# Performance work log

Hardware: AMD Instinct MI355X
Metric: run time of the kernel (lower is better)

## Reference

```python
import jax, jax.numpy as jnp
import numpy as np

N_HEADS = 8
EMBED_DIM = 512
HEAD_DIM = EMBED_DIM // N_HEADS
INPUT_DIM = 512


def setup_inputs() -> dict:
    key = jax.random.key(0)
    ks = jax.random.split(key, 9)
    B, N = 4, 2048
    s_in = 1.0 / np.sqrt(INPUT_DIM)
    s_e = 1.0 / np.sqrt(EMBED_DIM)
    return {
        "q": jax.random.normal(ks[0], (B, N, INPUT_DIM), dtype=jnp.float32),
        "wq": jax.random.uniform(ks[1], (EMBED_DIM, INPUT_DIM), jnp.float32, -s_in, s_in),
        "bq": jax.random.uniform(ks[2], (EMBED_DIM,), jnp.float32, -s_in, s_in),
        "wk": jax.random.uniform(ks[3], (EMBED_DIM, INPUT_DIM), jnp.float32, -s_in, s_in),
        "bk": jax.random.uniform(ks[4], (EMBED_DIM,), jnp.float32, -s_in, s_in),
        "wv": jax.random.uniform(ks[5], (EMBED_DIM, INPUT_DIM), jnp.float32, -s_in, s_in),
        "bv": jax.random.uniform(ks[6], (EMBED_DIM,), jnp.float32, -s_in, s_in),
        "wo": jax.random.uniform(ks[7], (EMBED_DIM, EMBED_DIM), jnp.float32, -s_e, s_e),
        "bo": jax.random.uniform(ks[8], (EMBED_DIM,), jnp.float32, -s_e, s_e),
    }


def reference(q, wq, bq, wk, bk, wv, bv, wo, bo):
    B, N, _ = q.shape
    # linear projections (torch Linear: x @ W.T + b)
    Q = (q @ wq.T + bq).reshape(B, N, N_HEADS, HEAD_DIM).transpose(0, 2, 1, 3)
    K = (q @ wk.T + bk).reshape(B, N, N_HEADS, HEAD_DIM).transpose(0, 2, 1, 3)
    V = (q @ wv.T + bv).reshape(B, N, N_HEADS, HEAD_DIM).transpose(0, 2, 1, 3)
    scores = jnp.einsum("bhqd,bhkd->bhqk", Q, K) / jnp.sqrt(
        jnp.asarray(HEAD_DIM, dtype=q.dtype)
    )
    weights = jax.nn.softmax(scores, axis=-1)
    out = jnp.einsum("bhqk,bhkd->bhqd", weights, V)  # [B,H,N,Dh]
    out = out.transpose(0, 2, 1, 3).reshape(B, N, EMBED_DIM)
    return out @ wo.T + bo
```

## Files before the change

### kernel.cpp

```cpp
#include <hip/hip_runtime.h>
#include <hip/hip_bf16.h>
#include <math.h>

#define SEQ    2048
#define DH     64
#define EMB    512
#define INDIM  512
#define NHEADS 8
#define BATCH  4
#define MTOT   (BATCH * SEQ)

typedef __attribute__((ext_vector_type(8))) short bf16x8;
typedef __attribute__((ext_vector_type(4))) float f32x4;

__device__ __forceinline__ ushort f2bf(float x) {
  union { float f; unsigned u; } v; v.f = x;
  unsigned r = v.u + 0x7FFFu + ((v.u >> 16) & 1u);
  return (ushort)(r >> 16);
}

__device__ __forceinline__ unsigned cvt_pk_bf16(float lo, float hi) {
  unsigned r;
  asm("v_cvt_pk_bf16_f32 %0, %1, %2" : "=v"(r) : "v"(lo), "v"(hi));
  return r;
}

__global__ __launch_bounds__(256) void conv_bf16(const float* __restrict__ src,
                                                 ushort* __restrict__ dst, int n8) {
  const int i = blockIdx.x * 256 + threadIdx.x;
  if (i >= n8) return;
  const float4 a = ((const float4*)src)[i * 2];
  const float4 b = ((const float4*)src)[i * 2 + 1];
  uint4 o;
  o.x = cvt_pk_bf16(a.x, a.y);
  o.y = cvt_pk_bf16(a.z, a.w);
  o.z = cvt_pk_bf16(b.x, b.y);
  o.w = cvt_pk_bf16(b.z, b.w);
  ((uint4*)dst)[i] = o;
}

__global__ __launch_bounds__(256) void conv_bf16_w4(
    const float* __restrict__ w0, const float* __restrict__ w1,
    const float* __restrict__ w2, const float* __restrict__ w3,
    ushort* __restrict__ dst, int n8per) {
  const int i = blockIdx.x * 256 + threadIdx.x;
  if (i >= n8per) return;
  const float* src = (blockIdx.y == 0) ? w0 : (blockIdx.y == 1) ? w1
                   : (blockIdx.y == 2) ? w2 : w3;
  ushort* d = dst + (size_t)blockIdx.y * n8per * 8;
  const float4 a = ((const float4*)src)[i * 2];
  const float4 b = ((const float4*)src)[i * 2 + 1];
  uint4 o;
  o.x = cvt_pk_bf16(a.x, a.y);
  o.y = cvt_pk_bf16(a.z, a.w);
  o.z = cvt_pk_bf16(b.x, b.y);
  o.w = cvt_pk_bf16(b.z, b.w);
  ((uint4*)d)[i] = o;
}

template <int MODE>
__global__ __launch_bounds__(256) void mfma_gemm(
    const ushort* __restrict__ A, const ushort* __restrict__ W,
    const float* __restrict__ b0, const float* __restrict__ b1,
    const float* __restrict__ b2,
    ushort* __restrict__ outQ, ushort* __restrict__ outK,
    ushort* __restrict__ outVT, float* __restrict__ outF) {
  __shared__ __align__(16) char smem[MODE == 0 ? 35840 : 16384];
  ushort* As = (ushort*)smem;
  ushort* Bs = (ushort*)(smem + 8192);
  ushort* Tl = (ushort*)smem;

  const int bm = blockIdx.x * 128;
  const int bn = blockIdx.y * 128;
  const int tid = threadIdx.x;
  const int wave = tid >> 6, lane = tid & 63;
  const int g = lane >> 4, ln = lane & 15;
  const int wr = wave >> 1, wc = wave & 1;

  f32x4 acc[4][4];
#pragma unroll
  for (int m = 0; m < 4; ++m)
#pragma unroll
    for (int n = 0; n < 4; ++n) acc[m][n] = (f32x4){0.f, 0.f, 0.f, 0.f};

  const size_t a_base = (size_t)(bm + wave * 16 + (lane >> 2)) * INDIM + (lane & 3) * 8;
  const size_t b_base = (size_t)(bn + wave * 16 + (lane >> 2)) * INDIM + (lane & 3) * 8;
  ushort* ldsA0 = As + wave * 512;
  ushort* ldsA1 = As + 2048 + wave * 512;
  ushort* ldsB0 = Bs + wave * 512;
  ushort* ldsB1 = Bs + 2048 + wave * 512;

  for (int k0 = 0; k0 < INDIM; k0 += 32) {
    __syncthreads();
    __builtin_amdgcn_global_load_lds(
        (const __attribute__((address_space(1))) void*)(A + a_base + k0),
        (__attribute__((address_space(3))) void*)ldsA0, 16, 0, 0);
    __builtin_amdgcn_global_load_lds(
        (const __attribute__((address_space(1))) void*)(A + a_base + 64 * INDIM + k0),
        (__attribute__((address_space(3))) void*)ldsA1, 16, 0, 0);
    __builtin_amdgcn_global_load_lds(
        (const __attribute__((address_space(1))) void*)(W + b_base + k0),
        (__attribute__((address_space(3))) void*)ldsB0, 16, 0, 0);
    __builtin_amdgcn_global_load_lds(
        (const __attribute__((address_space(1))) void*)(W + b_base + 64 * INDIM + k0),
        (__attribute__((address_space(3))) void*)ldsB1, 16, 0, 0);
    __syncthreads();

    bf16x8 af[4], bfv[4];
#pragma unroll
    for (int m = 0; m < 4; ++m)
      af[m] = *(const bf16x8*)&As[(64 * wr + 16 * m + ln) * 32 + 8 * g];
#pragma unroll
    for (int n = 0; n < 4; ++n)
      bfv[n] = *(const bf16x8*)&Bs[(64 * wc + 16 * n + ln) * 32 + 8 * g];
#pragma unroll
    for (int m = 0; m < 4; ++m)
#pragma unroll
      for (int n = 0; n < 4; ++n)
        acc[m][n] = __builtin_amdgcn_mfma_f32_16x16x32_bf16(af[m], bfv[n], acc[m][n], 0, 0, 0);
  }

  if (MODE == 1) {
#pragma unroll
    for (int n = 0; n < 4; ++n) {
      const int e = bn + 64 * wc + 16 * n + ln;
      const float bv = b0[e];
#pragma unroll
      for (int m = 0; m < 4; ++m)
#pragma unroll
        for (int r = 0; r < 4; ++r) {
          const int row = bm + 64 * wr + 16 * m + 4 * g + r;
          outF[(size_t)row * EMB + e] = acc[m][n][r] + bv;
        }
    }
    return;
  }

  const int which = bn >> 9;
  const float* bias = (which == 0) ? b0 : (which == 1) ? b1 : b2;

  if (which < 2) {
    const float scl = (which == 0) ? 0.18033688f : 1.0f;
    ushort* dst = (which == 0) ? outQ : outK;
#pragma unroll
    for (int n = 0; n < 4; ++n) {
      const int e = (bn & 511) + 64 * wc + 16 * n + ln;
      const float bv = bias[e];
      const int h = e >> 6, d = e & 63;
#pragma unroll
      for (int m = 0; m < 4; ++m)
#pragma unroll
        for (int r = 0; r < 4; ++r) {
          const int row = bm + 64 * wr + 16 * m + 4 * g + r;
          const int b = row >> 11, nn = row & (SEQ - 1);
          dst[(((size_t)(b * NHEADS + h) * SEQ) + nn) * DH + d] =
              f2bf((acc[m][n][r] + bv) * scl);
        }
    }
  } else {
    __syncthreads();
#pragma unroll
    for (int n = 0; n < 4; ++n) {
      const int cl = 64 * wc + 16 * n + ln;
      const float bv = bias[(bn & 511) + cl];
#pragma unroll
      for (int m = 0; m < 4; ++m)
#pragma unroll
        for (int r = 0; r < 4; ++r) {
          const int rl = 64 * wr + 16 * m + 4 * g + r;
          Tl[cl * 140 + rl] = f2bf(acc[m][n][r] + bv);
        }
    }
    __syncthreads();
    const int c = tid >> 1;
    const int rh = (tid & 1) * 64;
    const int e = (bn & 511) + c;
    const int h = e >> 6, d = e & 63;
    const int b = bm >> 11;
    const int nn0 = (bm & (SEQ - 1)) + rh;
    ushort* drow = outVT + (((size_t)(b * NHEADS + h) * DH) + d) * SEQ + nn0;
#pragma unroll
    for (int j = 0; j < 8; ++j)
      *(bf16x8*)&drow[j * 8] = *(const bf16x8*)&Tl[c * 140 + rh + j * 8];
  }
}

__global__ __launch_bounds__(256) void attn_mfma(const ushort* __restrict__ Q,
                                                 const ushort* __restrict__ K,
                                                 const ushort* __restrict__ VT,
                                                 ushort* __restrict__ O) {
  __shared__ __align__(16) ushort Kl[64 * 72];
  __shared__ __align__(16) ushort Vl[80 * 72];
  __shared__ __align__(16) ushort Pl[4][32 * 72];
  __shared__ float Sl[4][32];

  const int tid = threadIdx.x;
  const int wave = tid >> 6, lane = tid & 63;
  const int g = lane >> 4, ln = lane & 15;

  const int orig = blockIdx.y * gridDim.x + blockIdx.x;
  const int swz = (orig & 7) * 64 + (orig >> 3);
  const int bh = swz >> 4;
  const int qx = swz & 15;
  const int qbase = qx * 128 + wave * 32;

  for (int i = tid; i < 16 * 72; i += 256)
    Vl[64 * 72 + i] = (i < 72) ? (ushort)0x3F80 : (ushort)0;

  const ushort* Qb = Q + ((size_t)bh * SEQ + qbase) * DH;
  const ushort* Kb = K + (size_t)bh * SEQ * DH;
  const ushort* Vb = VT + (size_t)bh * DH * SEQ;

  const bf16x8 qfA0 = *(const bf16x8*)&Qb[ln * DH + 8 * g];
  const bf16x8 qfA1 = *(const bf16x8*)&Qb[ln * DH + 32 + 8 * g];
  const bf16x8 qfB0 = *(const bf16x8*)&Qb[(16 + ln) * DH + 8 * g];
  const bf16x8 qfB1 = *(const bf16x8*)&Qb[(16 + ln) * DH + 32 + 8 * g];

  f32x4 oaccA[5], oaccB[5];
#pragma unroll
  for (int t = 0; t < 5; ++t) {
    oaccA[t] = (f32x4){0.f, 0.f, 0.f, 0.f};
    oaccB[t] = (f32x4){0.f, 0.f, 0.f, 0.f};
  }

  const int skv = tid >> 3, sd = (tid & 7) * 8;
  const int dt = tid >> 2, kc = (tid & 3) * 8;

  bf16x8 k0v = *(const bf16x8*)&Kb[(size_t)skv * DH + sd];
  bf16x8 k1v = *(const bf16x8*)&Kb[(size_t)(32 + skv) * DH + sd];
  bf16x8 v0v = *(const bf16x8*)&Vb[(size_t)dt * SEQ + kc];
  bf16x8 v1v = *(const bf16x8*)&Vb[(size_t)dt * SEQ + 32 + kc];

  for (int kv0 = 0; kv0 < SEQ; kv0 += 64) {
    __syncthreads();
    *(bf16x8*)&Kl[skv * 72 + sd] = k0v;
    *(bf16x8*)&Kl[(32 + skv) * 72 + sd] = k1v;
    *(bf16x8*)&Vl[dt * 72 + kc] = v0v;
    *(bf16x8*)&Vl[dt * 72 + 32 + kc] = v1v;

    const int nxt = (kv0 + 64 < SEQ) ? kv0 + 64 : kv0;
    k0v = *(const bf16x8*)&Kb[(size_t)(nxt + skv) * DH + sd];
    k1v = *(const bf16x8*)&Kb[(size_t)(nxt + 32 + skv) * DH + sd];
    v0v = *(const bf16x8*)&Vb[(size_t)dt * SEQ + nxt + kc];
    v1v = *(const bf16x8*)&Vb[(size_t)dt * SEQ + nxt + 32 + kc];

    asm volatile("s_waitcnt lgkmcnt(0)" ::: "memory");
    __builtin_amdgcn_s_barrier();

    f32x4 saccA[4], saccB[4];
    __builtin_amdgcn_s_setprio(1);
#pragma unroll
    for (int t = 0; t < 4; ++t) {
      saccA[t] = (f32x4){0.f, 0.f, 0.f, 0.f};
      saccB[t] = (f32x4){0.f, 0.f, 0.f, 0.f};
      const bf16x8 ka0 = *(const bf16x8*)&Kl[(16 * t + ln) * 72 + 8 * g];
      const bf16x8 ka1 = *(const bf16x8*)&Kl[(16 * t + ln) * 72 + 32 + 8 * g];
      saccA[t] = __builtin_amdgcn_mfma_f32_16x16x32_bf16(ka0, qfA0, saccA[t], 0, 0, 0);
      saccA[t] = __builtin_amdgcn_mfma_f32_16x16x32_bf16(ka1, qfA1, saccA[t], 0, 0, 0);
      saccB[t] = __builtin_amdgcn_mfma_f32_16x16x32_bf16(ka0, qfB0, saccB[t], 0, 0, 0);
      saccB[t] = __builtin_amdgcn_mfma_f32_16x16x32_bf16(ka1, qfB1, saccB[t], 0, 0, 0);
    }
    __builtin_amdgcn_s_setprio(0);

    ushort* Pw = Pl[wave];
#pragma unroll
    for (int t = 0; t < 4; ++t) {
      uint2 pkA, pkB;
      pkA.x = cvt_pk_bf16(exp2f(saccA[t][0]), exp2f(saccA[t][1]));
      pkA.y = cvt_pk_bf16(exp2f(saccA[t][2]), exp2f(saccA[t][3]));
      pkB.x = cvt_pk_bf16(exp2f(saccB[t][0]), exp2f(saccB[t][1]));
      pkB.y = cvt_pk_bf16(exp2f(saccB[t][2]), exp2f(saccB[t][3]));
      *(uint2*)&Pw[ln * 72 + 16 * t + 4 * g] = pkA;
      *(uint2*)&Pw[(16 + ln) * 72 + 16 * t + 4 * g] = pkB;
    }

    __builtin_amdgcn_s_setprio(1);
#pragma unroll
    for (int c = 0; c < 2; ++c) {
      const bf16x8 paA = *(const bf16x8*)&Pw[ln * 72 + 32 * c + 8 * g];
      const bf16x8 paB = *(const bf16x8*)&Pw[(16 + ln) * 72 + 32 * c + 8 * g];
#pragma unroll
      for (int t = 0; t < 5; ++t) {
        const bf16x8 vb = *(const bf16x8*)&Vl[(16 * t + ln) * 72 + 32 * c + 8 * g];
        oaccA[t] = __builtin_amdgcn_mfma_f32_16x16x32_bf16(paA, vb, oaccA[t], 0, 0, 0);
        oaccB[t] = __builtin_amdgcn_mfma_f32_16x16x32_bf16(paB, vb, oaccB[t], 0, 0, 0);
      }
    }
    __builtin_amdgcn_s_setprio(0);
  }

  if (ln == 0) {
#pragma unroll
    for (int r = 0; r < 4; ++r) {
      Sl[wave][4 * g + r] = oaccA[4][r];
      Sl[wave][16 + 4 * g + r] = oaccB[4][r];
    }
  }
  const float invlA = 1.0f / Sl[wave][ln];
  const float invlB = 1.0f / Sl[wave][16 + ln];

  const int b = bh >> 3, h = bh & 7;
#pragma unroll
  for (int r = 0; r < 4; ++r) {
    const float irA = __shfl(invlA, 4 * g + r);
    const float irB = __shfl(invlB, 4 * g + r);
    ushort* opA = O + ((size_t)(b * SEQ) + qbase + 4 * g + r) * EMB + h * 64;
    ushort* opB = O + ((size_t)(b * SEQ) + qbase + 16 + 4 * g + r) * EMB + h * 64;
#pragma unroll
    for (int t = 0; t < 4; ++t) {
      opA[16 * t + ln] = f2bf(oaccA[t][r] * irA);
      opB[16 * t + ln] = f2bf(oaccB[t][r] * irB);
    }
  }
}

extern "C" void kernel_launch(void* const* d_in, const int* in_sizes, int n_in,
                              void* d_out, int out_size, void* d_ws, size_t ws_size,
                              hipStream_t stream) {
  const float* q  = (const float*)d_in[0];
  const float* wq = (const float*)d_in[1];
  const float* bq = (const float*)d_in[2];
  const float* wk = (const float*)d_in[3];
  const float* bk = (const float*)d_in[4];
  const float* wv = (const float*)d_in[5];
  const float* bv = (const float*)d_in[6];
  const float* wo = (const float*)d_in[7];
  const float* bo = (const float*)d_in[8];
  float* out = (float*)d_out;

  const size_t XSZ = (size_t)MTOT * INDIM;
  const size_t WSZ = (size_t)EMB * INDIM;
  const size_t QSZ = (size_t)BATCH * NHEADS * SEQ * DH;
  ushort* wsX = (ushort*)d_ws;
  ushort* wsW = wsX + XSZ;
  ushort* wsQ = wsW + 4 * WSZ;
  ushort* wsK = wsQ + QSZ;
  ushort* wsVT = wsK + QSZ;
  ushort* wsA = wsVT + QSZ;

  const dim3 blk(256);

  conv_bf16<<<dim3(XSZ / 8 / 256), blk, 0, stream>>>(q, wsX, XSZ / 8);
  conv_bf16_w4<<<dim3(WSZ / 8 / 256, 4), blk, 0, stream>>>(wq, wk, wv, wo, wsW, WSZ / 8);

  mfma_gemm<0><<<dim3(MTOT / 128, 1536 / 128), blk, 0, stream>>>(
      wsX, wsW, bq, bk, bv, wsQ, wsK, wsVT, nullptr);

  attn_mfma<<<dim3(SEQ / 128, BATCH * NHEADS), blk, 0, stream>>>(wsQ, wsK, wsVT, wsA);

  mfma_gemm<1><<<dim3(MTOT / 128, EMB / 128), blk, 0, stream>>>(
      wsA, wsW + 3 * WSZ, bo, nullptr, nullptr, nullptr, nullptr, nullptr, out);
}
```

Before: 115.0 us.

## Split attention KV range across two blocks with atomic partial-sum reduction

The attention grid doubles from 512 to 1024 blocks by giving each block half of the key/value sequence. Unnormalized outputs and row sums are accumulated into fp32 workspace buffers with atomicAdd, and a new normalize_o kernel divides and converts the result to bf16. This works without a running max because the softmax takes no max-subtraction. The aim is more parallelism to fill the GPU's compute units, paid for with a memset, float atomics over an 8192x512 buffer, and an extra kernel pass. The exp2f call is also swapped for a raw v_exp_f32 instruction.

```diff
diff --git a/kernel.cpp b/kernel.cpp
--- a/kernel.cpp
+++ b/kernel.cpp
@@ -22,6 +22,12 @@
 __device__ __forceinline__ unsigned cvt_pk_bf16(float lo, float hi) {
   unsigned r;
   asm("v_cvt_pk_bf16_f32 %0, %1, %2" : "=v"(r) : "v"(lo), "v"(hi));
+  return r;
+}
+
+__device__ __forceinline__ float fast_exp2(float x) {
+  float r;
+  asm("v_exp_f32 %0, %1" : "=v"(r) : "v"(x));
   return r;
 }
 
@@ -188,21 +194,24 @@
 __global__ __launch_bounds__(256) void attn_mfma(const ushort* __restrict__ Q,
                                                  const ushort* __restrict__ K,
                                                  const ushort* __restrict__ VT,
-                                                 ushort* __restrict__ O) {
+                                                 float* __restrict__ P,
+                                                 float* __restrict__ L) {
   __shared__ __align__(16) ushort Kl[64 * 72];
   __shared__ __align__(16) ushort Vl[80 * 72];
   __shared__ __align__(16) ushort Pl[4][32 * 72];
-  __shared__ float Sl[4][32];
 
   const int tid = threadIdx.x;
   const int wave = tid >> 6, lane = tid & 63;
   const int g = lane >> 4, ln = lane & 15;
 
   const int orig = blockIdx.y * gridDim.x + blockIdx.x;
-  const int swz = (orig & 7) * 64 + (orig >> 3);
-  const int bh = swz >> 4;
-  const int qx = swz & 15;
+  const int swz = (orig & 7) * 128 + (orig >> 3);
+  const int bh = swz >> 5;
+  const int sub = swz & 31;
+  const int qx = sub >> 1;
+  const int half = sub & 1;
   const int qbase = qx * 128 + wave * 32;
+  const int kvbeg = half << 10;
 
   for (int i = tid; i < 16 * 72; i += 256)
     Vl[64 * 72 + i] = (i < 72) ? (ushort)0x3F80 : (ushort)0;
@@ -226,23 +235,28 @@
   const int skv = tid >> 3, sd = (tid & 7) * 8;
   const int dt = tid >> 2, kc = (tid & 3) * 8;
 
-  bf16x8 k0v = *(const bf16x8*)&Kb[(size_t)skv * DH + sd];
-  bf16x8 k1v = *(const bf16x8*)&Kb[(size_t)(32 + skv) * DH + sd];
-  bf16x8 v0v = *(const bf16x8*)&Vb[(size_t)dt * SEQ + kc];
-  bf16x8 v1v = *(const bf16x8*)&Vb[(size_t)dt * SEQ + 32 + kc];
-
-  for (int kv0 = 0; kv0 < SEQ; kv0 += 64) {
+  const ushort* kp0 = Kb + (size_t)(kvbeg + skv) * DH + sd;
+  const ushort* kp1 = kp0 + 32 * DH;
+  const ushort* vp0 = Vb + (size_t)dt * SEQ + kvbeg + kc;
+  const ushort* vp1 = vp0 + 32;
+
+  bf16x8 k0v = *(const bf16x8*)kp0;
+  bf16x8 k1v = *(const bf16x8*)kp1;
+  bf16x8 v0v = *(const bf16x8*)vp0;
+  bf16x8 v1v = *(const bf16x8*)vp1;
+
+  for (int it = 0; it < 16; ++it) {
     __syncthreads();
     *(bf16x8*)&Kl[skv * 72 + sd] = k0v;
     *(bf16x8*)&Kl[(32 + skv) * 72 + sd] = k1v;
     *(bf16x8*)&Vl[dt * 72 + kc] = v0v;
     *(bf16x8*)&Vl[dt * 72 + 32 + kc] = v1v;
 
-    const int nxt = (kv0 + 64 < SEQ) ? kv0 + 64 : kv0;
-    k0v = *(const bf16x8*)&Kb[(size_t)(nxt + skv) * DH + sd];
-    k1v = *(const bf16x8*)&Kb[(size_t)(nxt + 32 + skv) * DH + sd];
-    v0v = *(const bf16x8*)&Vb[(size_t)dt * SEQ + nxt + kc];
-    v1v = *(const bf16x8*)&Vb[(size_t)dt * SEQ + nxt + 32 + kc];
+    kp0 += 64 * DH; kp1 += 64 * DH; vp0 += 64; vp1 += 64;
+    k0v = *(const bf16x8*)kp0;
+    k1v = *(const bf16x8*)kp1;
+    v0v = *(const bf16x8*)vp0;
+    v1v = *(const bf16x8*)vp1;
 
     asm volatile("s_waitcnt lgkmcnt(0)" ::: "memory");
     __builtin_amdgcn_s_barrier();
@@ -266,10 +280,10 @@
 #pragma unroll
     for (int t = 0; t < 4; ++t) {
       uint2 pkA, pkB;
-      pkA.x = cvt_pk_bf16(exp2f(saccA[t][0]), exp2f(saccA[t][1]));
-      pkA.y = cvt_pk_bf16(exp2f(saccA[t][2]), exp2f(saccA[t][3]));
-      pkB.x = cvt_pk_bf16(exp2f(saccB[t][0]), exp2f(saccB[t][1]));
-      pkB.y = cvt_pk_bf16(exp2f(saccB[t][2]), exp2f(saccB[t][3]));
+      pkA.x = cvt_pk_bf16(fast_exp2(saccA[t][0]), fast_exp2(saccA[t][1]));
+      pkA.y = cvt_pk_bf16(fast_exp2(saccA[t][2]), fast_exp2(saccA[t][3]));
+      pkB.x = cvt_pk_bf16(fast_exp2(saccB[t][0]), fast_exp2(saccB[t][1]));
+      pkB.y = cvt_pk_bf16(fast_exp2(saccB[t][2]), fast_exp2(saccB[t][3]));
       *(uint2*)&Pw[ln * 72 + 16 * t + 4 * g] = pkA;
       *(uint2*)&Pw[(16 + ln) * 72 + 16 * t + 4 * g] = pkB;
     }
@@ -289,29 +303,42 @@
     __builtin_amdgcn_s_setprio(0);
   }
 
+  const int b = bh >> 3, h = bh & 7;
+#pragma unroll
+  for (int r = 0; r < 4; ++r) {
+    float* opA = P + (size_t)(b * SEQ + qbase + 4 * g + r) * EMB + h * 64;
+    float* opB = opA + (size_t)16 * EMB;
+#pragma unroll
+    for (int t = 0; t < 4; ++t) {
+      atomicAdd(&opA[16 * t + ln], oaccA[t][r]);
+      atomicAdd(&opB[16 * t + ln], oaccB[t][r]);
+    }
+  }
   if (ln == 0) {
 #pragma unroll
     for (int r = 0; r < 4; ++r) {
-      Sl[wave][4 * g + r] = oaccA[4][r];
-      Sl[wave][16 + 4 * g + r] = oaccB[4][r];
-    }
-  }
-  const float invlA = 1.0f / Sl[wave][ln];
-  const float invlB = 1.0f / Sl[wave][16 + ln];
-
-  const int b = bh >> 3, h = bh & 7;
-#pragma unroll
-  for (int r = 0; r < 4; ++r) {
-    const float irA = __shfl(invlA, 4 * g + r);
-    const float irB = __shfl(invlB, 4 * g + r);
-    ushort* opA = O + ((size_t)(b * SEQ) + qbase + 4 * g + r) * EMB + h * 64;
-    ushort* opB = O + ((size_t)(b * SEQ) + qbase + 16 + 4 * g + r) * EMB + h * 64;
-#pragma unroll
-    for (int t = 0; t < 4; ++t) {
-      opA[16 * t + ln] = f2bf(oaccA[t][r] * irA);
-      opB[16 * t + ln] = f2bf(oaccB[t][r] * irB);
-    }
-  }
+      atomicAdd(&L[(size_t)(b * SEQ + qbase + 4 * g + r) * NHEADS + h], oaccA[4][r]);
+      atomicAdd(&L[(size_t)(b * SEQ + qbase + 16 + 4 * g + r) * NHEADS + h], oaccB[4][r]);
+    }
+  }
+}
+
+__global__ __launch_bounds__(256) void normalize_o(const float* __restrict__ P,
+                                                   const float* __restrict__ L,
+                                                   ushort* __restrict__ A) {
+  const int i = blockIdx.x * 256 + threadIdx.x;
+  const int row = i >> 6;
+  const int c = (i & 63) * 8;
+  const int h = c >> 6;
+  const float inv = 1.0f / L[(size_t)row * NHEADS + h];
+  const float4 p0 = *(const float4*)&P[(size_t)row * EMB + c];
+  const float4 p1 = *(const float4*)&P[(size_t)row * EMB + c + 4];
+  uint4 o;
+  o.x = cvt_pk_bf16(p0.x * inv, p0.y * inv);
+  o.y = cvt_pk_bf16(p0.z * inv, p0.w * inv);
+  o.z = cvt_pk_bf16(p1.x * inv, p1.y * inv);
+  o.w = cvt_pk_bf16(p1.z * inv, p1.w * inv);
+  ((uint4*)A)[i] = o;
 }
 
 extern "C" void kernel_launch(void* const* d_in, const int* in_sizes, int n_in,
@@ -336,7 +363,9 @@
   ushort* wsQ = wsW + 4 * WSZ;
   ushort* wsK = wsQ + QSZ;
   ushort* wsVT = wsK + QSZ;
-  ushort* wsA = wsVT + QSZ;
+  float*  wsP = (float*)(wsVT + QSZ);
+  float*  wsL = wsP + (size_t)MTOT * EMB;
+  ushort* wsA = wsQ;
 
   const dim3 blk(256);
 
@@ -346,7 +375,12 @@
   mfma_gemm<0><<<dim3(MTOT / 128, 1536 / 128), blk, 0, stream>>>(
       wsX, wsW, bq, bk, bv, wsQ, wsK, wsVT, nullptr);
 
-  attn_mfma<<<dim3(SEQ / 128, BATCH * NHEADS), blk, 0, stream>>>(wsQ, wsK, wsVT, wsA);
+  hipMemsetAsync(wsP, 0, (size_t)MTOT * EMB * sizeof(float) +
+                          (size_t)MTOT * NHEADS * sizeof(float), stream);
+
+  attn_mfma<<<dim3(32, 32), blk, 0, stream>>>(wsQ, wsK, wsVT, wsP, wsL);
+
+  normalize_o<<<dim3(MTOT * EMB / 8 / 256), blk, 0, stream>>>(wsP, wsL, wsA);
 
   mfma_gemm<1><<<dim3(MTOT / 128, EMB / 128), blk, 0, stream>>>(
       wsA, wsW + 3 * WSZ, bo, nullptr, nullptr, nullptr, nullptr, nullptr, out);
```

Measured after the change: 132.6 us. 15.4% more time.

## Keep softmax probabilities in registers via permlane swap instead of LDS round-trip

Applied to the files above, without the earlier changes.

The attention kernel no longer writes exp'd scores to a per-wave LDS buffer and reads them back as MFMA A-operands. Instead it packs them to bf16 and rearranges them across lanes with v_permlane32_swap, feeding the P·V MFMA straight from registers. The row-sum denominator, previously obtained by appending a ones row to V (a fifth MFMA tile), is now a register reduction with shuffles. It also permutes K rows in LDS so the score layout matches, uses raw v_exp_f32, and preloads the K/V fragments. This removes LDS traffic and one extra MFMA tile per step, at the cost of more register pressure and a fragile lane-mapping that must be exact.

```diff
diff --git a/kernel.cpp b/kernel.cpp
--- a/kernel.cpp
+++ b/kernel.cpp
@@ -23,6 +23,16 @@
   unsigned r;
   asm("v_cvt_pk_bf16_f32 %0, %1, %2" : "=v"(r) : "v"(lo), "v"(hi));
   return r;
+}
+
+__device__ __forceinline__ float fast_exp2(float x) {
+  float r;
+  asm("v_exp_f32 %0, %1" : "=v"(r) : "v"(x));
+  return r;
+}
+
+__device__ __forceinline__ void permswap32(unsigned &x, unsigned &y) {
+  asm("v_permlane32_swap_b32 %0, %1" : "+v"(x), "+v"(y));
 }
 
 __global__ __launch_bounds__(256) void conv_bf16(const float* __restrict__ src,
@@ -190,23 +200,18 @@
                                                  const ushort* __restrict__ VT,
                                                  ushort* __restrict__ O) {
   __shared__ __align__(16) ushort Kl[64 * 72];
-  __shared__ __align__(16) ushort Vl[80 * 72];
-  __shared__ __align__(16) ushort Pl[4][32 * 72];
-  __shared__ float Sl[4][32];
+  __shared__ __align__(16) ushort Vl[64 * 72];
 
   const int tid = threadIdx.x;
   const int wave = tid >> 6, lane = tid & 63;
   const int g = lane >> 4, ln = lane & 15;
 
-  const int orig = blockIdx.y * gridDim.x + blockIdx.x;
+  const int orig = blockIdx.x;
   const int swz = (orig & 7) * 64 + (orig >> 3);
   const int bh = swz >> 4;
   const int qx = swz & 15;
   const int qbase = qx * 128 + wave * 32;
 
-  for (int i = tid; i < 16 * 72; i += 256)
-    Vl[64 * 72 + i] = (i < 72) ? (ushort)0x3F80 : (ushort)0;
-
   const ushort* Qb = Q + ((size_t)bh * SEQ + qbase) * DH;
   const ushort* Kb = K + (size_t)bh * SEQ * DH;
   const ushort* Vb = VT + (size_t)bh * DH * SEQ;
@@ -216,15 +221,19 @@
   const bf16x8 qfB0 = *(const bf16x8*)&Qb[(16 + ln) * DH + 8 * g];
   const bf16x8 qfB1 = *(const bf16x8*)&Qb[(16 + ln) * DH + 32 + 8 * g];
 
-  f32x4 oaccA[5], oaccB[5];
-#pragma unroll
-  for (int t = 0; t < 5; ++t) {
+  f32x4 oaccA[4], oaccB[4];
+#pragma unroll
+  for (int t = 0; t < 4; ++t) {
     oaccA[t] = (f32x4){0.f, 0.f, 0.f, 0.f};
     oaccB[t] = (f32x4){0.f, 0.f, 0.f, 0.f};
   }
+  float denomA = 0.f, denomB = 0.f;
 
   const int skv = tid >> 3, sd = (tid & 7) * 8;
   const int dt = tid >> 2, kc = (tid & 3) * 8;
+  const int pr0 = skv ^ (((((skv >> 2) ^ (skv >> 3)) & 1)) * 12);
+  const int s32 = skv + 32;
+  const int pr1 = s32 ^ (((((s32 >> 2) ^ (s32 >> 3)) & 1)) * 12);
 
   bf16x8 k0v = *(const bf16x8*)&Kb[(size_t)skv * DH + sd];
   bf16x8 k1v = *(const bf16x8*)&Kb[(size_t)(32 + skv) * DH + sd];
@@ -233,8 +242,8 @@
 
   for (int kv0 = 0; kv0 < SEQ; kv0 += 64) {
     __syncthreads();
-    *(bf16x8*)&Kl[skv * 72 + sd] = k0v;
-    *(bf16x8*)&Kl[(32 + skv) * 72 + sd] = k1v;
+    *(bf16x8*)&Kl[pr0 * 72 + sd] = k0v;
+    *(bf16x8*)&Kl[pr1 * 72 + sd] = k1v;
     *(bf16x8*)&Vl[dt * 72 + kc] = v0v;
     *(bf16x8*)&Vl[dt * 72 + 32 + kc] = v1v;
 
@@ -247,63 +256,136 @@
     asm volatile("s_waitcnt lgkmcnt(0)" ::: "memory");
     __builtin_amdgcn_s_barrier();
 
-    f32x4 saccA[4], saccB[4];
-    __builtin_amdgcn_s_setprio(1);
+    bf16x8 ka[4][2], vb[2][4];
 #pragma unroll
     for (int t = 0; t < 4; ++t) {
-      saccA[t] = (f32x4){0.f, 0.f, 0.f, 0.f};
-      saccB[t] = (f32x4){0.f, 0.f, 0.f, 0.f};
-      const bf16x8 ka0 = *(const bf16x8*)&Kl[(16 * t + ln) * 72 + 8 * g];
-      const bf16x8 ka1 = *(const bf16x8*)&Kl[(16 * t + ln) * 72 + 32 + 8 * g];
-      saccA[t] = __builtin_amdgcn_mfma_f32_16x16x32_bf16(ka0, qfA0, saccA[t], 0, 0, 0);
-      saccA[t] = __builtin_amdgcn_mfma_f32_16x16x32_bf16(ka1, qfA1, saccA[t], 0, 0, 0);
-      saccB[t] = __builtin_amdgcn_mfma_f32_16x16x32_bf16(ka0, qfB0, saccB[t], 0, 0, 0);
-      saccB[t] = __builtin_amdgcn_mfma_f32_16x16x32_bf16(ka1, qfB1, saccB[t], 0, 0, 0);
-    }
-    __builtin_amdgcn_s_setprio(0);
-
-    ushort* Pw = Pl[wave];
-#pragma unroll
-    for (int t = 0; t < 4; ++t) {
-      uint2 pkA, pkB;
-      pkA.x = cvt_pk_bf16(exp2f(saccA[t][0]), exp2f(saccA[t][1]));
-      pkA.y = cvt_pk_bf16(exp2f(saccA[t][2]), exp2f(saccA[t][3]));
-      pkB.x = cvt_pk_bf16(exp2f(saccB[t][0]), exp2f(saccB[t][1]));
-      pkB.y = cvt_pk_bf16(exp2f(saccB[t][2]), exp2f(saccB[t][3]));
-      *(uint2*)&Pw[ln * 72 + 16 * t + 4 * g] = pkA;
-      *(uint2*)&Pw[(16 + ln) * 72 + 16 * t + 4 * g] = pkB;
-    }
-
-    __builtin_amdgcn_s_setprio(1);
-#pragma unroll
-    for (int c = 0; c < 2; ++c) {
-      const bf16x8 paA = *(const bf16x8*)&Pw[ln * 72 + 32 * c + 8 * g];
-      const bf16x8 paB = *(const bf16x8*)&Pw[(16 + ln) * 72 + 32 * c + 8 * g];
-#pragma unroll
-      for (int t = 0; t < 5; ++t) {
-        const bf16x8 vb = *(const bf16x8*)&Vl[(16 * t + ln) * 72 + 32 * c + 8 * g];
-        oaccA[t] = __builtin_amdgcn_mfma_f32_16x16x32_bf16(paA, vb, oaccA[t], 0, 0, 0);
-        oaccB[t] = __builtin_amdgcn_mfma_f32_16x16x32_bf16(paB, vb, oaccB[t], 0, 0, 0);
+      ka[t][0] = *(const bf16x8*)&Kl[(16 * t + ln) * 72 + 8 * g];
+      ka[t][1] = *(const bf16x8*)&Kl[(16 * t + ln) * 72 + 32 + 8 * g];
+    }
+#pragma unroll
+    for (int c = 0; c < 2; ++c)
+#pragma unroll
+      for (int t = 0; t < 4; ++t)
+        vb[c][t] = *(const bf16x8*)&Vl[(16 * t + ln) * 72 + 32 * c + 8 * g];
+
+    {
+      f32x4 s0 = (f32x4){0.f, 0.f, 0.f, 0.f};
+      f32x4 s1 = s0, s2 = s0, s3 = s0;
+      __builtin_amdgcn_s_setprio(1);
+      s0 = __builtin_amdgcn_mfma_f32_16x16x32_bf16(ka[0][0], qfA0, s0, 0, 0, 0);
+      s1 = __builtin_amdgcn_mfma_f32_16x16x32_bf16(ka[1][0], qfA0, s1, 0, 0, 0);
+      s2 = __builtin_amdgcn_mfma_f32_16x16x32_bf16(ka[2][0], qfA0, s2, 0, 0, 0);
+      s3 = __builtin_amdgcn_mfma_f32_16x16x32_bf16(ka[3][0], qfA0, s3, 0, 0, 0);
+      s0 = __builtin_amdgcn_mfma_f32_16x16x32_bf16(ka[0][1], qfA1, s0, 0, 0, 0);
+      s1 = __builtin_amdgcn_mfma_f32_16x16x32_bf16(ka[1][1], qfA1, s1, 0, 0, 0);
+      s2 = __builtin_amdgcn_mfma_f32_16x16x32_bf16(ka[2][1], qfA1, s2, 0, 0, 0);
+      s3 = __builtin_amdgcn_mfma_f32_16x16x32_bf16(ka[3][1], qfA1, s3, 0, 0, 0);
+      __builtin_amdgcn_s_setprio(0);
+
+      float p0[4], p1[4], p2[4], p3[4];
+#pragma unroll
+      for (int r = 0; r < 4; ++r) {
+        p0[r] = fast_exp2(s0[r]);
+        p1[r] = fast_exp2(s1[r]);
+        p2[r] = fast_exp2(s2[r]);
+        p3[r] = fast_exp2(s3[r]);
       }
-    }
-    __builtin_amdgcn_s_setprio(0);
-  }
-
-  if (ln == 0) {
-#pragma unroll
-    for (int r = 0; r < 4; ++r) {
-      Sl[wave][4 * g + r] = oaccA[4][r];
-      Sl[wave][16 + 4 * g + r] = oaccB[4][r];
-    }
-  }
-  const float invlA = 1.0f / Sl[wave][ln];
-  const float invlB = 1.0f / Sl[wave][16 + ln];
-
+      float ds = ((p0[0] + p0[1]) + (p0[2] + p0[3]))
+               + ((p1[0] + p1[1]) + (p1[2] + p1[3]))
+               + ((p2[0] + p2[1]) + (p2[2] + p2[3]))
+               + ((p3[0] + p3[1]) + (p3[2] + p3[3]));
+      ds += __shfl_xor(ds, 16);
+      ds += __shfl_xor(ds, 32);
+      denomA += ds;
+
+      unsigned a0 = cvt_pk_bf16(p0[0], p0[1]);
+      unsigned a2 = cvt_pk_bf16(p1[0], p1[1]);
+      unsigned a1 = cvt_pk_bf16(p0[2], p0[3]);
+      unsigned a3 = cvt_pk_bf16(p1[2], p1[3]);
+      permswap32(a0, a2);
+      permswap32(a1, a3);
+      unsigned b0 = cvt_pk_bf16(p2[0], p2[1]);
+      unsigned b2 = cvt_pk_bf16(p3[0], p3[1]);
+      unsigned b1 = cvt_pk_bf16(p2[2], p2[3]);
+      unsigned b3 = cvt_pk_bf16(p3[2], p3[3]);
+      permswap32(b0, b2);
+      permswap32(b1, b3);
+      union { unsigned u[4]; bf16x8 v; } pa0, pa1;
+      pa0.u[0] = a0; pa0.u[1] = a1; pa0.u[2] = a2; pa0.u[3] = a3;
+      pa1.u[0] = b0; pa1.u[1] = b1; pa1.u[2] = b2; pa1.u[3] = b3;
+
+      __builtin_amdgcn_s_setprio(1);
+#pragma unroll
+      for (int t = 0; t < 4; ++t) {
+        oaccA[t] = __builtin_amdgcn_mfma_f32_16x16x32_bf16(pa0.v, vb[0][t], oaccA[t], 0, 0, 0);
+        oaccA[t] = __builtin_amdgcn_mfma_f32_16x16x32_bf16(pa1.v, vb[1][t], oaccA[t], 0, 0, 0);
+      }
+      __builtin_amdgcn_s_setprio(0);
+    }
+
+    {
+      f32x4 s0 = (f32x4){0.f, 0.f, 0.f, 0.f};
+      f32x4 s1 = s0, s2 = s0, s3 = s0;
+      __builtin_amdgcn_s_setprio(1);
+      s0 = __builtin_amdgcn_mfma_f32_16x16x32_bf16(ka[0][0], qfB0, s0, 0, 0, 0);
+      s1 = __builtin_amdgcn_mfma_f32_16x16x32_bf16(ka[1][0], qfB0, s1, 0, 0, 0);
+      s2 = __builtin_amdgcn_mfma_f32_16x16x32_bf16(ka[2][0], qfB0, s2, 0, 0, 0);
+      s3 = __builtin_amdgcn_mfma_f32_16x16x32_bf16(ka[3][0], qfB0, s3, 0, 0, 0);
+      s0 = __builtin_amdgcn_mfma_f32_16x16x32_bf16(ka[0][1], qfB1, s0, 0, 0, 0);
+      s1 = __builtin_amdgcn_mfma_f32_16x16x32_bf16(ka[1][1], qfB1, s1, 0, 0, 0);
+      s2 = __builtin_amdgcn_mfma_f32_16x16x32_bf16(ka[2][1], qfB1, s2, 0, 0, 0);
+      s3 = __builtin_amdgcn_mfma_f32_16x16x32_bf16(ka[3][1], qfB1, s3, 0, 0, 0);
+      __builtin_amdgcn_s_setprio(0);
+
+      float p0[4], p1[4], p2[4], p3[4];
+#pragma unroll
+      for (int r = 0; r < 4; ++r) {
+        p0[r] = fast_exp2(s0[r]);
+        p1[r] = fast_exp2(s1[r]);
+        p2[r] = fast_exp2(s2[r]);
+        p3[r] = fast_exp2(s3[r]);
+      }
+      float ds = ((p0[0] + p0[1]) + (p0[2] + p0[3]))
+               + ((p1[0] + p1[1]) + (p1[2] + p1[3]))
+               + ((p2[0] + p2[1]) + (p2[2] + p2[3]))
+               + ((p3[0] + p3[1]) + (p3[2] + p3[3]));
+      ds += __shfl_xor(ds, 16);
+      ds += __shfl_xor(ds, 32);
+      denomB += ds;
+
+      unsigned a0 = cvt_pk_bf16(p0[0], p0[1]);
+      unsigned a2 = cvt_pk_bf16(p1[0], p1[1]);
+      unsigned a1 = cvt_pk_bf16(p0[2], p0[3]);
+      unsigned a3 = cvt_pk_bf16(p1[2], p1[3]);
+      permswap32(a0, a2);
+      permswap32(a1, a3);
+      unsigned b0 = cvt_pk_bf16(p2[0], p2[1]);
+      unsigned b2 = cvt_pk_bf16(p3[0], p3[1]);
+      unsigned b1 = cvt_pk_bf16(p2[2], p2[3]);
+      unsigned b3 = cvt_pk_bf16(p3[2], p3[3]);
+      permswap32(b0, b2);
+      permswap32(b1, b3);
+      union { unsigned u[4]; bf16x8 v; } pa0, pa1;
+      pa0.u[0] = a0; pa0.u[1] = a1; pa0.u[2] = a2; pa0.u[3] = a3;
+      pa1.u[0] = b0; pa1.u[1] = b1; pa1.u[2] = b2; pa1.u[3] = b3;
+
+      __builtin_amdgcn_s_setprio(1);
+#pragma unroll
+      for (int t = 0; t < 4; ++t) {
+        oaccB[t] = __builtin_amdgcn_mfma_f32_16x16x32_bf16(pa0.v, vb[0][t], oaccB[t], 0, 0, 0);
+        oaccB[t] = __builtin_amdgcn_mfma_f32_16x16x32_bf16(pa1.v, vb[1][t], oaccB[t], 0, 0, 0);
+      }
+      __builtin_amdgcn_s_setprio(0);
+    }
+  }
+
+  const float invA = 1.0f / denomA;
+  const float invB = 1.0f / denomB;
   const int b = bh >> 3, h = bh & 7;
 #pragma unroll
   for (int r = 0; r < 4; ++r) {
-    const float irA = __shfl(invlA, 4 * g + r);
-    const float irB = __shfl(invlB, 4 * g + r);
+    const float irA = __shfl(invA, 4 * g + r);
+    const float irB = __shfl(invB, 4 * g + r);
     ushort* opA = O + ((size_t)(b * SEQ) + qbase + 4 * g + r) * EMB + h * 64;
     ushort* opB = O + ((size_t)(b * SEQ) + qbase + 16 + 4 * g + r) * EMB + h * 64;
 #pragma unroll
@@ -346,7 +428,7 @@
   mfma_gemm<0><<<dim3(MTOT / 128, 1536 / 128), blk, 0, stream>>>(
       wsX, wsW, bq, bk, bv, wsQ, wsK, wsVT, nullptr);
 
-  attn_mfma<<<dim3(SEQ / 128, BATCH * NHEADS), blk, 0, stream>>>(wsQ, wsK, wsVT, wsA);
+  attn_mfma<<<dim3(512), blk, 0, stream>>>(wsQ, wsK, wsVT, wsA);
 
   mfma_gemm<1><<<dim3(MTOT / 128, EMB / 128), blk, 0, stream>>>(
       wsA, wsW + 3 * WSZ, bo, nullptr, nullptr, nullptr, nullptr, nullptr, out);
```

Result: faster. 107.6 us (-6.4%).
